# Optimization experiments

Measured on AMD Instinct MI355X. Metric: run time of the kernel, lower is better.

The kernel has to match this reference:

```python
import jax, jax.numpy as jnp
import numpy as np

B = 16        # num graphs
N = 256       # nodes per graph
EMB = 16      # rrwp feature dim (K random-walk steps)
OUT = 64      # output edge-attr dim
E_SPARSE = 65536  # observed sparse edges (avg degree 16)


def _full_pairs(num_graphs, n):
    g = jnp.arange(num_graphs)
    r = jnp.arange(n)
    src = jnp.broadcast_to(g[:, None, None] * n + r[None, :, None], (num_graphs, n, n)).reshape(-1)
    dst = jnp.broadcast_to(g[:, None, None] * n + r[None, None, :], (num_graphs, n, n)).reshape(-1)
    return src, dst


def setup_inputs() -> dict:
    key = jax.random.key(0)
    k1, k2, k3, k4, k5, k6 = jax.random.split(key, 6)
    # RRWP covers all intra-graph node pairs (relative random-walk probs)
    src, dst = _full_pairs(B, N)
    rrwp_index = jnp.stack([src, dst])
    rrwp_val = jax.random.normal(k1, (B * N * N, EMB), dtype=jnp.float32)
    # sparse observed edges: random intra-graph pairs
    eg = jax.random.randint(k2, (E_SPARSE,), 0, B)
    er = jax.random.randint(k3, (E_SPARSE,), 0, N)
    ec = jax.random.randint(k4, (E_SPARSE,), 0, N)
    edge_index = jnp.stack([eg * N + er, eg * N + ec])
    edge_attr = jax.random.normal(k5, (E_SPARSE, OUT), dtype=jnp.float32)
    batch = jnp.repeat(jnp.arange(B), N)
    # xavier-uniform init of fc weight [out_dim, emb_dim]
    limit = float(np.sqrt(6.0 / (EMB + OUT)))
    W = jax.random.uniform(k6, (OUT, EMB), minval=-limit, maxval=limit, dtype=jnp.float32)
    return {
        "rrwp_index": rrwp_index, "rrwp_val": rrwp_val,
        "edge_index": edge_index, "edge_attr": edge_attr,
        "batch": batch, "W": W,
        "num_nodes": B * N, "num_graphs": B,
    }


def reference(rrwp_index, rrwp_val, edge_index, edge_attr, batch, W, num_nodes, num_graphs):
    # Equal-size graphs: graph id = node // n, local id = node % n.
    n = num_nodes // num_graphs
    out_dim = W.shape[0]

    def flat(idx):  # [2,E] global node pairs -> row index in dense per-graph full edge list
        g = idx[0] // n
        return (g * n + idx[0] % n) * n + (idx[1] % n)

    # FC_1(RRWP); fc has no bias
    vals = rrwp_val @ W.T  # [E_rrwp, out_dim]

    # pad_to_full_graph with fill_value=0 and zero-attr self loops =>
    # final coalesced values are scatter-add of all contributions onto the
    # dense (row-major sorted, per-graph) full edge list.
    dense = jnp.zeros((num_graphs * n * n, out_dim), dtype=vals.dtype)
    dense = dense.at[flat(rrwp_index)].add(vals)
    dense = dense.at[flat(edge_index)].add(edge_attr)

    g = jnp.arange(num_graphs)
    r = jnp.arange(n)
    src = jnp.broadcast_to(g[:, None, None] * n + r[None, :, None], (num_graphs, n, n)).reshape(-1)
    dst = jnp.broadcast_to(g[:, None, None] * n + r[None, None, :], (num_graphs, n, n)).reshape(-1)
    out_idx = jnp.stack([src, dst])  # matches torch_sparse.coalesce sorted order
    return out_idx, dense
```

## Files before the change

### kernel.cpp

```cpp
#include <hip/hip_runtime.h>
#include <stdint.h>

#define E_RRWP 1048576
#define ES     65536
#define NNODES 4096

__global__ __launch_bounds__(256) void k_idx(float* __restrict__ out) {
    int t = blockIdx.x * 256 + threadIdx.x;
    int p = t * 8;
    float s = (float)(p >> 8);
    float4 sv = make_float4(s, s, s, s);
    ((float4*)out)[t * 2]     = sv;
    ((float4*)out)[t * 2 + 1] = sv;
    int dbase = ((p >> 16) << 8) | (p & 255);
    ((float4*)(out + E_RRWP))[t * 2] =
        make_float4((float)dbase, (float)(dbase + 1), (float)(dbase + 2), (float)(dbase + 3));
    ((float4*)(out + E_RRWP))[t * 2 + 1] =
        make_float4((float)(dbase + 4), (float)(dbase + 5), (float)(dbase + 6), (float)(dbase + 7));
}

__global__ __launch_bounds__(256) void k_dense(
    const float* __restrict__ xv,
    const float* __restrict__ Wf,
    float* __restrict__ dense)
{
    __shared__ float Wt[16][64];
    int tid = threadIdx.x;
    {
        float4 wv = ((const float4*)Wf)[tid];
        int d = tid >> 2, k0 = (tid & 3) * 4;
        Wt[k0 + 0][d] = wv.x;
        Wt[k0 + 1][d] = wv.y;
        Wt[k0 + 2][d] = wv.z;
        Wt[k0 + 3][d] = wv.w;
    }
    __syncthreads();

    int dg = tid & 15;
    int rg = tid >> 4;
    size_t row0 = (size_t)blockIdx.x * 128 + rg * 8;

    float4 w[16];
#pragma unroll
    for (int k = 0; k < 16; k++)
        w[k] = *(const float4*)&Wt[k][dg * 4];

#pragma unroll
    for (int r = 0; r < 8; r++) {
        const float4* xr = (const float4*)(xv + (row0 + r) * 16);
        float4 x0 = xr[0], x1 = xr[1], x2 = xr[2], x3 = xr[3];
        float xk[16] = { x0.x, x0.y, x0.z, x0.w, x1.x, x1.y, x1.z, x1.w,
                         x2.x, x2.y, x2.z, x2.w, x3.x, x3.y, x3.z, x3.w };
        float a0 = 0.f, a1 = 0.f, a2 = 0.f, a3 = 0.f;
#pragma unroll
        for (int k = 0; k < 16; k++) {
            a0 += xk[k] * w[k].x;
            a1 += xk[k] * w[k].y;
            a2 += xk[k] * w[k].z;
            a3 += xk[k] * w[k].w;
        }
        ((float4*)dense)[(row0 + r) * 16 + dg] = make_float4(a0, a1, a2, a3);
    }
}

__global__ __launch_bounds__(256) void k_sparse(
    const int* __restrict__ ei,
    const float* __restrict__ ea,
    float* __restrict__ dense)
{
    int t = blockIdx.x * 256 + threadIdx.x;
    int e = t >> 4, j = t & 15;
    unsigned s = (unsigned)ei[e];
    unsigned d = (unsigned)ei[ES + e];
    if (s >= (unsigned)NNODES || d >= (unsigned)NNODES) return;
    unsigned flat = (s << 8) | (d & 255u);

    float4 a = ((const float4*)ea)[(size_t)e * 16 + j];
    float* p = dense + (size_t)flat * 64 + j * 4;
    atomicAdd(p + 0, a.x);
    atomicAdd(p + 1, a.y);
    atomicAdd(p + 2, a.z);
    atomicAdd(p + 3, a.w);
}

extern "C" void kernel_launch(void* const* d_in, const int* in_sizes, int n_in,
                              void* d_out, int out_size, void* d_ws, size_t ws_size,
                              hipStream_t stream) {
    const float* rrwp_val   = (const float*)d_in[1];
    const int*   edge_index = (const int*)d_in[2];
    const float* edge_attr  = (const float*)d_in[3];
    const float* W          = (const float*)d_in[5];

    float* out   = (float*)d_out;
    float* dense = out + 2 * E_RRWP;

    k_idx<<<E_RRWP / 8 / 256, 256, 0, stream>>>(out);
    k_dense<<<E_RRWP / 128, 256, 0, stream>>>(rrwp_val, W, dense);
    k_sparse<<<ES * 16 / 256, 256, 0, stream>>>(edge_index, edge_attr, dense);
}
```

Baseline: 424.5 us.

## Replace atomic scatter with per-row linked lists gathered inside dense GEMM kernel

```diff
diff --git a/kernel.cpp b/kernel.cpp
--- a/kernel.cpp
+++ b/kernel.cpp
@@ -5,27 +5,50 @@
 #define ES     65536
 #define NNODES 4096
 
-__global__ __launch_bounds__(256) void k_idx(float* __restrict__ out) {
+
+__global__ __launch_bounds__(256) void k_zero(uint4* __restrict__ head4) {
     int t = blockIdx.x * 256 + threadIdx.x;
-    int p = t * 8;
-    float s = (float)(p >> 8);
-    float4 sv = make_float4(s, s, s, s);
-    ((float4*)out)[t * 2]     = sv;
-    ((float4*)out)[t * 2 + 1] = sv;
-    int dbase = ((p >> 16) << 8) | (p & 255);
-    ((float4*)(out + E_RRWP))[t * 2] =
-        make_float4((float)dbase, (float)(dbase + 1), (float)(dbase + 2), (float)(dbase + 3));
-    ((float4*)(out + E_RRWP))[t * 2 + 1] =
-        make_float4((float)(dbase + 4), (float)(dbase + 5), (float)(dbase + 6), (float)(dbase + 7));
+    head4[t] = make_uint4(0u, 0u, 0u, 0u);
 }
 
-__global__ __launch_bounds__(256) void k_dense(
+__global__ __launch_bounds__(256) void k_build(
+    const int* __restrict__ ei,
+    unsigned* __restrict__ head,
+    unsigned* __restrict__ nxt)
+{
+    int e = blockIdx.x * 256 + threadIdx.x;
+    unsigned s = (unsigned)ei[e];
+    unsigned d = (unsigned)ei[ES + e];
+    if (s >= (unsigned)NNODES || d >= (unsigned)NNODES) return;
+    unsigned flat = (s << 8) | (d & 255u);
+    nxt[e] = atomicExch(&head[flat], (unsigned)(e + 1));
+}
+
+__global__ __launch_bounds__(256) void k_main(
     const float* __restrict__ xv,
     const float* __restrict__ Wf,
+    const float* __restrict__ ea,
+    const unsigned* __restrict__ head,
+    const unsigned* __restrict__ nxt,
+    float* __restrict__ outIdx,
     float* __restrict__ dense)
 {
     __shared__ float Wt[16][64];
     int tid = threadIdx.x;
+    int p0  = blockIdx.x * 128;
+
+    if (tid < 64) {
+        if (tid < 32) {
+            float s = (float)(p0 >> 8);
+            ((float4*)outIdx)[(p0 >> 2) + tid] = make_float4(s, s, s, s);
+        } else {
+            int tt = tid - 32;
+            int d0 = (((p0 >> 16) << 8) | (p0 & 255)) + tt * 4;
+            ((float4*)(outIdx + E_RRWP))[(p0 >> 2) + tt] =
+                make_float4((float)d0, (float)(d0 + 1), (float)(d0 + 2), (float)(d0 + 3));
+        }
+    }
+
     {
         float4 wv = ((const float4*)Wf)[tid];
         int d = tid >> 2, k0 = (tid & 3) * 4;
@@ -38,12 +61,16 @@
 
     int dg = tid & 15;
     int rg = tid >> 4;
-    size_t row0 = (size_t)blockIdx.x * 128 + rg * 8;
+    size_t row0 = (size_t)p0 + rg * 8;
 
     float4 w[16];
 #pragma unroll
     for (int k = 0; k < 16; k++)
         w[k] = *(const float4*)&Wt[k][dg * 4];
+
+    uint4 h0 = ((const uint4*)(head + row0))[0];
+    uint4 h1 = ((const uint4*)(head + row0))[1];
+    unsigned h[8] = { h0.x, h0.y, h0.z, h0.w, h1.x, h1.y, h1.z, h1.w };
 
 #pragma unroll
     for (int r = 0; r < 8; r++) {
@@ -59,28 +86,12 @@
             a2 += xk[k] * w[k].z;
             a3 += xk[k] * w[k].w;
         }
+        for (unsigned x = h[r]; x != 0u; x = nxt[x - 1]) {
+            float4 av = ((const float4*)ea)[(size_t)(x - 1) * 16 + dg];
+            a0 += av.x; a1 += av.y; a2 += av.z; a3 += av.w;
+        }
         ((float4*)dense)[(row0 + r) * 16 + dg] = make_float4(a0, a1, a2, a3);
     }
-}
-
-__global__ __launch_bounds__(256) void k_sparse(
-    const int* __restrict__ ei,
-    const float* __restrict__ ea,
-    float* __restrict__ dense)
-{
-    int t = blockIdx.x * 256 + threadIdx.x;
-    int e = t >> 4, j = t & 15;
-    unsigned s = (unsigned)ei[e];
-    unsigned d = (unsigned)ei[ES + e];
-    if (s >= (unsigned)NNODES || d >= (unsigned)NNODES) return;
-    unsigned flat = (s << 8) | (d & 255u);
-
-    float4 a = ((const float4*)ea)[(size_t)e * 16 + j];
-    float* p = dense + (size_t)flat * 64 + j * 4;
-    atomicAdd(p + 0, a.x);
-    atomicAdd(p + 1, a.y);
-    atomicAdd(p + 2, a.z);
-    atomicAdd(p + 3, a.w);
 }
 
 extern "C" void kernel_launch(void* const* d_in, const int* in_sizes, int n_in,
@@ -94,7 +105,11 @@
     float* out   = (float*)d_out;
     float* dense = out + 2 * E_RRWP;
 
-    k_idx<<<E_RRWP / 8 / 256, 256, 0, stream>>>(out);
-    k_dense<<<E_RRWP / 128, 256, 0, stream>>>(rrwp_val, W, dense);
-    k_sparse<<<ES * 16 / 256, 256, 0, stream>>>(edge_index, edge_attr, dense);
+    unsigned* head = (unsigned*)d_ws;
+    unsigned* nxt  = head + E_RRWP;
+
+    k_zero <<<E_RRWP / 4 / 256, 256, 0, stream>>>((uint4*)head);
+    k_build<<<ES / 256,          256, 0, stream>>>(edge_index, head, nxt);
+    k_main <<<E_RRWP / 128,      256, 0, stream>>>(rrwp_val, W, edge_attr,
+                                                   head, nxt, out, dense);
 }
```

Result: faster. 401.9 us (-5.3%).
